# Kernel optimization log

Hardware: AMD Instinct MI355X
Metric: run time of the kernel (lower is better)

## Reference

```python
import jax, jax.numpy as jnp
import numpy as np

B, L, D = 16, 4096, 256
DEP = 50


def setup_inputs() -> dict:
    key = jax.random.key(0)
    ks = jax.random.split(key, 20)
    s = 1.0 / np.sqrt(D)
    inp = {
        "inputs": jax.random.normal(ks[0], (B, L, D), jnp.float32),
        "parent_positions": jax.random.randint(ks[1], (B, L), 0, L, jnp.int32),
        "sentence_deps": jax.random.randint(ks[2], (B, L), 0, DEP, jnp.int32),
        "attention_mask": jax.random.randint(ks[3], (B, L), 0, 2, jnp.int32),
        # linear weights stored [in, out]
        "W_loop": jax.random.uniform(ks[4], (D, D), jnp.float32, -s, s),
        "b_loop": jnp.zeros((D,), jnp.float32),
        "W_child": jax.random.uniform(ks[5], (D, D), jnp.float32, -s, s),
        "b_child": jnp.zeros((D,), jnp.float32),
        "W_parent": jax.random.uniform(ks[6], (D, D), jnp.float32, -s, s),
        "b_parent": jnp.zeros((D,), jnp.float32),
        "w_loop_g": jax.random.uniform(ks[7], (D, 1), jnp.float32, -s, s),
        "b_loop_g": jnp.zeros((1,), jnp.float32),
        "w_child_g": jax.random.uniform(ks[8], (D, 1), jnp.float32, -s, s),
        "b_child_g": jnp.zeros((1,), jnp.float32),
        "w_parent_g": jax.random.uniform(ks[9], (D, 1), jnp.float32, -s, s),
        "b_parent_g": jnp.zeros((1,), jnp.float32),
        "E_pw": jax.random.normal(ks[10], (DEP, D), jnp.float32),
        "E_cw": jax.random.normal(ks[11], (DEP, D), jnp.float32),
        "E_pg": jax.random.normal(ks[12], (DEP, 1), jnp.float32),
        "E_cg": jax.random.normal(ks[13], (DEP, 1), jnp.float32),
    }
    return inp


def _scatter_add_children(idx, vals):
    # idx: [L] parent index per child; vals: [L, D]
    # out[p] = sum_{i: idx[i]==p} vals[i]  (== one_hot(idx).T @ vals)
    return jnp.zeros((L, vals.shape[-1]), vals.dtype).at[idx].add(vals)


def reference(inputs, parent_positions, sentence_deps, attention_mask,
              W_loop, b_loop, W_child, b_child, W_parent, b_parent,
              w_loop_g, b_loop_g, w_child_g, b_child_g, w_parent_g, b_parent_g,
              E_pw, E_cw, E_pg, E_cg):
    x = inputs
    n_iterator = 1
    for _ in range(n_iterator):
        # gather parent node states: [B, L, D]
        par = jnp.take_along_axis(x, parent_positions[:, :, None].astype(jnp.int32), axis=1)
        deps = sentence_deps
        loop_gate = jax.nn.sigmoid(x @ w_loop_g + b_loop_g)                       # [B,L,1]
        par_gate = jax.nn.sigmoid(x @ w_parent_g + b_parent_g + E_pg[deps])       # [B,L,1]
        child_gate = jax.nn.sigmoid(x @ w_child_g + b_child_g + E_cg[deps])       # [B,L,1]
        loop_conv = loop_gate * (x @ W_loop + b_loop)
        parent_conv = par_gate * (par @ W_parent + b_parent + E_pw[deps])
        child_mat = child_gate * (x @ W_child + b_child + E_cw[deps])
        # masked parents (pad positions point to 0), then scatter-add children
        mpp = jnp.where(attention_mask != 0, parent_positions, 0)
        child_conv = jax.vmap(_scatter_add_children)(mpp, child_mat)
        x = loop_conv + parent_conv + child_conv
    return x * attention_mask[:, :, None].astype(x.dtype)
```

## Files before the change

kernel.cpp:

```cpp
#include <hip/hip_runtime.h>
#include <hip/hip_bf16.h>
#include <stdint.h>

#define B_ 16
#define L_ 4096
#define D_ 256
#define M_ (B_*L_)
#define N_ 768

typedef __attribute__((ext_vector_type(8))) short bf16x8;
typedef __attribute__((ext_vector_type(4))) float f32x4;
typedef __attribute__((ext_vector_type(4))) int i32x4;

__device__ __forceinline__ float bf2f(unsigned short u) {
  union { unsigned int i; float f; } v; v.i = ((unsigned int)u) << 16; return v.f;
}
__device__ __forceinline__ unsigned short f2bf(float f) {
  __hip_bfloat16 h = __float2bfloat16(f);
  return *reinterpret_cast<unsigned short*>(&h);
}
__device__ __forceinline__ void async16(const void* g, void* l) {
  __builtin_amdgcn_global_load_lds((const __attribute__((address_space(1))) void*)g,
                                   (__attribute__((address_space(3))) void*)l, 16, 0, 0);
}
__device__ __forceinline__ float sigmoidf_(float z) {
  return 1.f / (1.f + __expf(-z));
}

__global__ __launch_bounds__(256) void k_pre(
    const float* __restrict__ x, const int* __restrict__ deps,
    const int* __restrict__ parent, const int* __restrict__ mask,
    const float* __restrict__ wlg, const float* __restrict__ blg,
    const float* __restrict__ wcg, const float* __restrict__ bcg,
    const float* __restrict__ wpg, const float* __restrict__ bpg,
    const float* __restrict__ Epg, const float* __restrict__ Ecg,
    const float* __restrict__ Wl, const float* __restrict__ Wp,
    const float* __restrict__ Wc,
    unsigned short* __restrict__ xb, float4* __restrict__ gates,
    unsigned short* __restrict__ WbT,
    int* __restrict__ cnt, int* __restrict__ off, int* __restrict__ lists)
{
  __shared__ int hist[4096];
  __shared__ int tot[256];
  const int bx = blockIdx.x;
  const int tid = threadIdx.x;

  if (bx >= 2048) {
    if (bx < 2816) {
      const int n = bx - 2048;
      const float* W = (n < 256) ? Wl : ((n < 512) ? Wp : Wc);
      WbT[(size_t)n * 256 + tid] = f2bf(W[(size_t)tid * 256 + (n & 255)]);
    } else {
      const int b = bx - 2816;
      const int base = b << 12;
      #pragma unroll
      for (int j = 0; j < 16; ++j) hist[tid + j * 256] = 0;
      __syncthreads();
      for (int j = 0; j < 16; ++j) {
        const int i = base + j * 256 + tid;
        if (mask[i]) {
          const int p = parent[i];
          if (p > 0 && mask[base + p]) atomicAdd(&hist[p], 1);
        }
      }
      __syncthreads();
      int v[16], s = 0;
      #pragma unroll
      for (int j = 0; j < 16; ++j) { v[j] = hist[tid * 16 + j]; s += v[j]; }
      tot[tid] = s;
      __syncthreads();
      for (int o = 1; o < 256; o <<= 1) {
        int xx = (tid >= o) ? tot[tid - o] : 0;
        __syncthreads();
        tot[tid] += xx;
        __syncthreads();
      }
      int run = tot[tid] - s;
      #pragma unroll
      for (int j = 0; j < 16; ++j) {
        const int k = tid * 16 + j;
        cnt[base + k] = v[j];
        off[base + k] = run;
        hist[k] = run;
        run += v[j];
      }
      __syncthreads();
      for (int j = 0; j < 16; ++j) {
        const int i = base + j * 256 + tid;
        if (mask[i]) {
          const int p = parent[i];
          if (p > 0 && mask[base + p]) {
            const int pos = atomicAdd(&hist[p], 1);
            lists[base + pos] = i;
          }
        }
      }
    }
    return;
  }

  const int lane = tid & 63;
  const int gw = (bx * 256 + tid) >> 6;
  const float4 wl4 = ((const float4*)wlg)[lane];
  const float4 wc4 = ((const float4*)wcg)[lane];
  const float4 wp4 = ((const float4*)wpg)[lane];
  const float bl0 = blg[0], bc0 = bcg[0], bp0 = bpg[0];
  for (int t = 0; t < 8; ++t) {
    const int i = gw * 8 + t;
    float4 xv = ((const float4*)x)[(size_t)i * 64 + lane];
    float sl = xv.x * wl4.x + xv.y * wl4.y + xv.z * wl4.z + xv.w * wl4.w;
    float sc = xv.x * wc4.x + xv.y * wc4.y + xv.z * wc4.z + xv.w * wc4.w;
    float sp = xv.x * wp4.x + xv.y * wp4.y + xv.z * wp4.z + xv.w * wp4.w;
    #pragma unroll
    for (int o = 32; o; o >>= 1) {
      sl += __shfl_xor(sl, o);
      sc += __shfl_xor(sc, o);
      sp += __shfl_xor(sp, o);
    }
    ushort4 u;
    u.x = f2bf(xv.x); u.y = f2bf(xv.y); u.z = f2bf(xv.z); u.w = f2bf(xv.w);
    ((ushort4*)xb)[(size_t)i * 64 + lane] = u;
    if (lane == 0) {
      int d = deps[i];
      float gl = sigmoidf_(sl + bl0);
      float gp = sigmoidf_(sp + bp0 + Epg[d]);
      float gc = sigmoidf_(sc + bc0 + Ecg[d]);
      gates[i] = make_float4(gl, gp, gc, 0.f);
    }
  }
}

__global__ __launch_bounds__(256) void k_gemm(
    const unsigned short* __restrict__ A,
    const unsigned short* __restrict__ Bt,
    unsigned short* __restrict__ Y)
{
  __shared__ unsigned short sh[2 * 128 * 64];
  unsigned short* lA = sh;
  unsigned short* lB = sh + 128 * 64;
  const int tid = threadIdx.x;
  const int wid = tid >> 6, lane = tid & 63;
  const int wm = wid >> 1, wn = wid & 1;
  const int bid = blockIdx.x;
  const int mb = bid / 6, nb = bid % 6;

  f32x4 acc[4][4] = {};
  const unsigned short* Ag = A + (size_t)mb * 128 * 256;
  const unsigned short* Bg = Bt + (size_t)nb * 128 * 256;
  const int srow = wid * 8 + (lane >> 3);
  const int scol = (lane & 7) * 8;

  for (int kb = 0; kb < 256; kb += 64) {
    #pragma unroll
    for (int s = 0; s < 4; ++s) {
      char* dA = (char*)lA + s * 4096 + wid * 1024 + lane * 16;
      char* dB = (char*)lB + s * 4096 + wid * 1024 + lane * 16;
      async16(Ag + (size_t)(s * 32 + srow) * 256 + kb + scol, dA);
      async16(Bg + (size_t)(s * 32 + srow) * 256 + kb + scol, dB);
    }
    __syncthreads();
    #pragma unroll
    for (int kk = 0; kk < 64; kk += 32) {
      const int ko = kk + (lane >> 4) * 8;
      bf16x8 af[4], bv[4];
      #pragma unroll
      for (int m = 0; m < 4; ++m)
        af[m] = *(const bf16x8*)&lA[(wm * 64 + m * 16 + (lane & 15)) * 64 + ko];
      #pragma unroll
      for (int n = 0; n < 4; ++n)
        bv[n] = *(const bf16x8*)&lB[(wn * 64 + n * 16 + (lane & 15)) * 64 + ko];
      #pragma unroll
      for (int m = 0; m < 4; ++m)
        #pragma unroll
        for (int n = 0; n < 4; ++n)
          acc[m][n] = __builtin_amdgcn_mfma_f32_16x16x32_bf16(af[m], bv[n], acc[m][n], 0, 0, 0);
    }
    __syncthreads();
  }

  #pragma unroll
  for (int m = 0; m < 4; ++m)
    #pragma unroll
    for (int n = 0; n < 4; ++n)
      #pragma unroll
      for (int r = 0; r < 4; ++r)
        sh[(wm * 64 + m * 16 + (lane >> 4) * 4 + r) * 128 + wn * 64 + n * 16 + (lane & 15)]
            = f2bf(acc[m][n][r]);
  __syncthreads();
  #pragma unroll
  for (int s = 0; s < 8; ++s) {
    const int o = s * 4096 + tid * 16;
    const int row = o >> 8;
    const int colu = (o & 255) >> 1;
    *(i32x4*)&Y[(size_t)(mb * 128 + row) * 768 + nb * 128 + colu] =
        *(const i32x4*)((const char*)sh + o);
  }
}

__global__ __launch_bounds__(256) void k_fused(
    const unsigned short* __restrict__ Y, const float4* __restrict__ gates,
    const int* __restrict__ parent, const int* __restrict__ deps,
    const int* __restrict__ mask, const int* __restrict__ cnt,
    const int* __restrict__ off, const int* __restrict__ lists,
    const float* __restrict__ b_loop, const float* __restrict__ b_parent,
    const float* __restrict__ b_child,
    const float* __restrict__ Epw, const float* __restrict__ Ecw,
    float* __restrict__ out)
{
  const int lane = threadIdx.x & 63;
  const int i = blockIdx.x * 4 + (threadIdx.x >> 6);
  const int b = i >> 12;
  float4* orow = (float4*)(out + (size_t)i * 256) + lane;
  if (!mask[i]) { *orow = make_float4(0.f, 0.f, 0.f, 0.f); return; }

  const float4 g = gates[i];
  const int p = parent[i], d = deps[i];
  const float4 bl = ((const float4*)b_loop)[lane];
  const float4 bp = ((const float4*)b_parent)[lane];
  const ushort4 yl = ((const ushort4*)(Y + (size_t)i * 768))[lane];
  const ushort4 z  = ((const ushort4*)(Y + (size_t)((b << 12) + p) * 768 + 256))[lane];
  const float4 e   = ((const float4*)Epw)[d * 64 + lane];
  float4 o;
  o.x = g.x * (bf2f(yl.x) + bl.x) + g.y * (bf2f(z.x) + bp.x + e.x);
  o.y = g.x * (bf2f(yl.y) + bl.y) + g.y * (bf2f(z.y) + bp.y + e.y);
  o.z = g.x * (bf2f(yl.z) + bl.z) + g.y * (bf2f(z.z) + bp.z + e.z);
  o.w = g.x * (bf2f(yl.w) + bl.w) + g.y * (bf2f(z.w) + bp.w + e.w);

  const int n = cnt[i];
  if (n) {
    const int o0 = off[i];
    const float4 bc = ((const float4*)b_child)[lane];
    for (int k = 0; k < n; ++k) {
      const int c = lists[(b << 12) + o0 + k];
      const float gc = ((const float*)gates)[c * 4 + 2];
      const int dc = deps[c];
      const ushort4 yc = ((const ushort4*)(Y + (size_t)c * 768 + 512))[lane];
      const float4 ec = ((const float4*)Ecw)[dc * 64 + lane];
      o.x += gc * (bf2f(yc.x) + bc.x + ec.x);
      o.y += gc * (bf2f(yc.y) + bc.y + ec.y);
      o.z += gc * (bf2f(yc.z) + bc.z + ec.z);
      o.w += gc * (bf2f(yc.w) + bc.w + ec.w);
    }
  }
  *orow = o;
}

__global__ __launch_bounds__(256) void k_row0(
    const unsigned short* __restrict__ Y, const float4* __restrict__ gates,
    const int* __restrict__ parent, const int* __restrict__ deps,
    const int* __restrict__ mask, const float* __restrict__ b_child,
    const float* __restrict__ Ecw, float* __restrict__ out)
{
  const int blk = blockIdx.x;
  const int b = blk >> 4;
  if (!mask[b << 12]) return;
  const int lane = threadIdx.x & 63;
  const int wid = threadIdx.x >> 6;
  const float4 bc = ((const float4*)b_child)[lane];
  float4 acc = make_float4(0.f, 0.f, 0.f, 0.f);
  const int tbase = (b << 12) + (blk & 15) * 256 + wid * 64;
  for (int t = 0; t < 64; ++t) {
    const int i = tbase + t;
    const int mi = mask[i];
    const int p = parent[i];
    if (mi && p != 0) continue;
    const float gc = ((const float*)gates)[i * 4 + 2];
    const int d = deps[i];
    const ushort4 yc = ((const ushort4*)(Y + (size_t)i * 768 + 512))[lane];
    const float4 ec = ((const float4*)Ecw)[d * 64 + lane];
    acc.x += gc * (bf2f(yc.x) + bc.x + ec.x);
    acc.y += gc * (bf2f(yc.y) + bc.y + ec.y);
    acc.z += gc * (bf2f(yc.z) + bc.z + ec.z);
    acc.w += gc * (bf2f(yc.w) + bc.w + ec.w);
  }
  __shared__ float4 red[4][64];
  red[wid][lane] = acc;
  __syncthreads();
  if (wid == 0) {
    float4 a0 = red[0][lane], a1 = red[1][lane], a2 = red[2][lane], a3 = red[3][lane];
    a0.x += a1.x + a2.x + a3.x;
    a0.y += a1.y + a2.y + a3.y;
    a0.z += a1.z + a2.z + a3.z;
    a0.w += a1.w + a2.w + a3.w;
    float* dst = out + (size_t)(b << 12) * 256 + lane * 4;
    unsafeAtomicAdd(dst + 0, a0.x);
    unsafeAtomicAdd(dst + 1, a0.y);
    unsafeAtomicAdd(dst + 2, a0.z);
    unsafeAtomicAdd(dst + 3, a0.w);
  }
}

extern "C" void kernel_launch(void* const* d_in, const int* in_sizes, int n_in,
                              void* d_out, int out_size, void* d_ws, size_t ws_size,
                              hipStream_t stream) {
  const float* x        = (const float*)d_in[0];
  const int*   parent   = (const int*)d_in[1];
  const int*   deps     = (const int*)d_in[2];
  const int*   mask     = (const int*)d_in[3];
  const float* W_loop   = (const float*)d_in[4];
  const float* b_loop   = (const float*)d_in[5];
  const float* W_child  = (const float*)d_in[6];
  const float* b_child  = (const float*)d_in[7];
  const float* W_parent = (const float*)d_in[8];
  const float* b_parent = (const float*)d_in[9];
  const float* wlg      = (const float*)d_in[10];
  const float* blg      = (const float*)d_in[11];
  const float* wcg      = (const float*)d_in[12];
  const float* bcg      = (const float*)d_in[13];
  const float* wpg      = (const float*)d_in[14];
  const float* bpg      = (const float*)d_in[15];
  const float* Epw      = (const float*)d_in[16];
  const float* Ecw      = (const float*)d_in[17];
  const float* Epg      = (const float*)d_in[18];
  const float* Ecg      = (const float*)d_in[19];
  float* out = (float*)d_out;

  char* ws = (char*)d_ws;
  unsigned short* xb  = (unsigned short*)ws;
  unsigned short* WbT = (unsigned short*)(ws + 33554432);
  float4* gates       = (float4*)(ws + 33947648);
  unsigned short* Yv  = (unsigned short*)(ws + 34996224);
  int* cnt            = (int*)(ws + 135659520);
  int* off            = (int*)(ws + 135921664);
  int* lists          = (int*)(ws + 136183808);

  k_pre<<<2832, 256, 0, stream>>>(x, deps, parent, mask, wlg, blg, wcg, bcg,
                                  wpg, bpg, Epg, Ecg, W_loop, W_parent, W_child,
                                  xb, gates, WbT, cnt, off, lists);
  k_gemm<<<3072, 256, 0, stream>>>(xb, WbT, Yv);
  k_fused<<<16384, 256, 0, stream>>>(Yv, gates, parent, deps, mask, cnt, off,
                                     lists, b_loop, b_parent, b_child,
                                     Epw, Ecw, out);
  k_row0<<<256, 256, 0, stream>>>(Yv, gates, parent, deps, mask, b_child,
                                  Ecw, out);
}
```

Measured before the change: 278.8 us.

## Merge row-0 kernel into fused pass, move child-list build into GEMM launch

The separate row-0 scatter kernel is folded into the fused kernel as extra blocks, and row 0 is now accumulated atomically after being zeroed by the GEMM kernel. The per-batch child histogram and list build moves from the prologue kernel into 16 extra blocks of the GEMM kernel. The weight transpose now handles four columns per block, and the gate shuffle reductions are batched across eight rows. This removes one launch and shortens the prologue, but it adds a cross-kernel ordering dependency for zeroing row 0 and makes row-0 output depend on atomics.

Result: faster. 267.8 us (-3.9%).

```diff
diff --git a/kernel.cpp b/kernel.cpp
--- a/kernel.cpp
+++ b/kernel.cpp
@@ -29,7 +29,6 @@
 
 __global__ __launch_bounds__(256) void k_pre(
     const float* __restrict__ x, const int* __restrict__ deps,
-    const int* __restrict__ parent, const int* __restrict__ mask,
     const float* __restrict__ wlg, const float* __restrict__ blg,
     const float* __restrict__ wcg, const float* __restrict__ bcg,
     const float* __restrict__ wpg, const float* __restrict__ bpg,
@@ -37,65 +36,20 @@
     const float* __restrict__ Wl, const float* __restrict__ Wp,
     const float* __restrict__ Wc,
     unsigned short* __restrict__ xb, float4* __restrict__ gates,
-    unsigned short* __restrict__ WbT,
-    int* __restrict__ cnt, int* __restrict__ off, int* __restrict__ lists)
+    unsigned short* __restrict__ WbT)
 {
-  __shared__ int hist[4096];
-  __shared__ int tot[256];
   const int bx = blockIdx.x;
   const int tid = threadIdx.x;
 
   if (bx >= 2048) {
-    if (bx < 2816) {
-      const int n = bx - 2048;
-      const float* W = (n < 256) ? Wl : ((n < 512) ? Wp : Wc);
-      WbT[(size_t)n * 256 + tid] = f2bf(W[(size_t)tid * 256 + (n & 255)]);
-    } else {
-      const int b = bx - 2816;
-      const int base = b << 12;
-      #pragma unroll
-      for (int j = 0; j < 16; ++j) hist[tid + j * 256] = 0;
-      __syncthreads();
-      for (int j = 0; j < 16; ++j) {
-        const int i = base + j * 256 + tid;
-        if (mask[i]) {
-          const int p = parent[i];
-          if (p > 0 && mask[base + p]) atomicAdd(&hist[p], 1);
-        }
-      }
-      __syncthreads();
-      int v[16], s = 0;
-      #pragma unroll
-      for (int j = 0; j < 16; ++j) { v[j] = hist[tid * 16 + j]; s += v[j]; }
-      tot[tid] = s;
-      __syncthreads();
-      for (int o = 1; o < 256; o <<= 1) {
-        int xx = (tid >= o) ? tot[tid - o] : 0;
-        __syncthreads();
-        tot[tid] += xx;
-        __syncthreads();
-      }
-      int run = tot[tid] - s;
-      #pragma unroll
-      for (int j = 0; j < 16; ++j) {
-        const int k = tid * 16 + j;
-        cnt[base + k] = v[j];
-        off[base + k] = run;
-        hist[k] = run;
-        run += v[j];
-      }
-      __syncthreads();
-      for (int j = 0; j < 16; ++j) {
-        const int i = base + j * 256 + tid;
-        if (mask[i]) {
-          const int p = parent[i];
-          if (p > 0 && mask[base + p]) {
-            const int pos = atomicAdd(&hist[p], 1);
-            lists[base + pos] = i;
-          }
-        }
-      }
-    }
+    const int n0 = (bx - 2048) * 4;
+    const float* W = (n0 < 256) ? Wl : ((n0 < 512) ? Wp : Wc);
+    const int c0 = n0 & 255;
+    const float4 v = *(const float4*)&W[(size_t)tid * 256 + c0];
+    WbT[(size_t)(n0 + 0) * 256 + tid] = f2bf(v.x);
+    WbT[(size_t)(n0 + 1) * 256 + tid] = f2bf(v.y);
+    WbT[(size_t)(n0 + 2) * 256 + tid] = f2bf(v.z);
+    WbT[(size_t)(n0 + 3) * 256 + tid] = f2bf(v.w);
     return;
   }
 
@@ -105,27 +59,35 @@
   const float4 wc4 = ((const float4*)wcg)[lane];
   const float4 wp4 = ((const float4*)wpg)[lane];
   const float bl0 = blg[0], bc0 = bcg[0], bp0 = bpg[0];
+  float sl[8], sc[8], sp[8];
+  #pragma unroll
   for (int t = 0; t < 8; ++t) {
     const int i = gw * 8 + t;
-    float4 xv = ((const float4*)x)[(size_t)i * 64 + lane];
-    float sl = xv.x * wl4.x + xv.y * wl4.y + xv.z * wl4.z + xv.w * wl4.w;
-    float sc = xv.x * wc4.x + xv.y * wc4.y + xv.z * wc4.z + xv.w * wc4.w;
-    float sp = xv.x * wp4.x + xv.y * wp4.y + xv.z * wp4.z + xv.w * wp4.w;
-    #pragma unroll
-    for (int o = 32; o; o >>= 1) {
-      sl += __shfl_xor(sl, o);
-      sc += __shfl_xor(sc, o);
-      sp += __shfl_xor(sp, o);
-    }
+    const float4 xv = ((const float4*)x)[(size_t)i * 64 + lane];
+    sl[t] = xv.x * wl4.x + xv.y * wl4.y + xv.z * wl4.z + xv.w * wl4.w;
+    sc[t] = xv.x * wc4.x + xv.y * wc4.y + xv.z * wc4.z + xv.w * wc4.w;
+    sp[t] = xv.x * wp4.x + xv.y * wp4.y + xv.z * wp4.z + xv.w * wp4.w;
     ushort4 u;
     u.x = f2bf(xv.x); u.y = f2bf(xv.y); u.z = f2bf(xv.z); u.w = f2bf(xv.w);
     ((ushort4*)xb)[(size_t)i * 64 + lane] = u;
-    if (lane == 0) {
-      int d = deps[i];
-      float gl = sigmoidf_(sl + bl0);
-      float gp = sigmoidf_(sp + bp0 + Epg[d]);
-      float gc = sigmoidf_(sc + bc0 + Ecg[d]);
-      gates[i] = make_float4(gl, gp, gc, 0.f);
+  }
+  #pragma unroll
+  for (int o = 32; o; o >>= 1) {
+    #pragma unroll
+    for (int t = 0; t < 8; ++t) {
+      sl[t] += __shfl_xor(sl[t], o);
+      sc[t] += __shfl_xor(sc[t], o);
+      sp[t] += __shfl_xor(sp[t], o);
+    }
+  }
+  if (lane == 0) {
+    #pragma unroll
+    for (int t = 0; t < 8; ++t) {
+      const int i = gw * 8 + t;
+      const int d = deps[i];
+      gates[i] = make_float4(sigmoidf_(sl[t] + bl0),
+                             sigmoidf_(sp[t] + bp0 + Epg[d]),
+                             sigmoidf_(sc[t] + bc0 + Ecg[d]), 0.f);
     }
   }
 }
@@ -133,15 +95,70 @@
 __global__ __launch_bounds__(256) void k_gemm(
     const unsigned short* __restrict__ A,
     const unsigned short* __restrict__ Bt,
-    unsigned short* __restrict__ Y)
+    unsigned short* __restrict__ Y,
+    const int* __restrict__ parent, const int* __restrict__ mask,
+    int* __restrict__ cnt, int* __restrict__ off, int* __restrict__ lists,
+    float* __restrict__ out)
 {
   __shared__ unsigned short sh[2 * 128 * 64];
+  const int tid = threadIdx.x;
+
+  if (blockIdx.x < 16) {
+    int* hist = (int*)sh;
+    int* tot = ((int*)sh) + 4096;
+    const int b = blockIdx.x;
+    const int base = b << 12;
+    out[(size_t)base * 256 + tid] = 0.f;
+    #pragma unroll
+    for (int j = 0; j < 16; ++j) hist[tid + j * 256] = 0;
+    __syncthreads();
+    for (int j = 0; j < 16; ++j) {
+      const int i = base + j * 256 + tid;
+      if (mask[i]) {
+        const int p = parent[i];
+        if (p > 0 && mask[base + p]) atomicAdd(&hist[p], 1);
+      }
+    }
+    __syncthreads();
+    int v[16], s = 0;
+    #pragma unroll
+    for (int j = 0; j < 16; ++j) { v[j] = hist[tid * 16 + j]; s += v[j]; }
+    tot[tid] = s;
+    __syncthreads();
+    for (int o = 1; o < 256; o <<= 1) {
+      int xx = (tid >= o) ? tot[tid - o] : 0;
+      __syncthreads();
+      tot[tid] += xx;
+      __syncthreads();
+    }
+    int run = tot[tid] - s;
+    #pragma unroll
+    for (int j = 0; j < 16; ++j) {
+      const int k = tid * 16 + j;
+      cnt[base + k] = v[j];
+      off[base + k] = run;
+      hist[k] = run;
+      run += v[j];
+    }
+    __syncthreads();
+    for (int j = 0; j < 16; ++j) {
+      const int i = base + j * 256 + tid;
+      if (mask[i]) {
+        const int p = parent[i];
+        if (p > 0 && mask[base + p]) {
+          const int pos = atomicAdd(&hist[p], 1);
+          lists[base + pos] = i;
+        }
+      }
+    }
+    return;
+  }
+
   unsigned short* lA = sh;
   unsigned short* lB = sh + 128 * 64;
-  const int tid = threadIdx.x;
   const int wid = tid >> 6, lane = tid & 63;
   const int wm = wid >> 1, wn = wid & 1;
-  const int bid = blockIdx.x;
+  const int bid = blockIdx.x - 16;
   const int mb = bid / 6, nb = bid % 6;
 
   f32x4 acc[4][4] = {};
@@ -208,10 +225,55 @@
     float* __restrict__ out)
 {
   const int lane = threadIdx.x & 63;
-  const int i = blockIdx.x * 4 + (threadIdx.x >> 6);
+  const int wid = threadIdx.x >> 6;
+
+  if (blockIdx.x >= 16384) {
+    const int blk = blockIdx.x - 16384;
+    const int b = blk >> 4;
+    if (!mask[b << 12]) return;
+    const float4 bc = ((const float4*)b_child)[lane];
+    float4 acc = make_float4(0.f, 0.f, 0.f, 0.f);
+    const int tbase = (b << 12) + (blk & 15) * 256 + wid * 64;
+    for (int t = 0; t < 64; ++t) {
+      const int i = tbase + t;
+      const int mi = mask[i];
+      const int p = parent[i];
+      if (mi && p != 0) continue;
+      const float gc = ((const float*)gates)[i * 4 + 2];
+      const int d = deps[i];
+      const ushort4 yc = ((const ushort4*)(Y + (size_t)i * 768 + 512))[lane];
+      const float4 ec = ((const float4*)Ecw)[d * 64 + lane];
+      acc.x += gc * (bf2f(yc.x) + bc.x + ec.x);
+      acc.y += gc * (bf2f(yc.y) + bc.y + ec.y);
+      acc.z += gc * (bf2f(yc.z) + bc.z + ec.z);
+      acc.w += gc * (bf2f(yc.w) + bc.w + ec.w);
+    }
+    __shared__ float4 red[4][64];
+    red[wid][lane] = acc;
+    __syncthreads();
+    if (wid == 0) {
+      float4 a0 = red[0][lane], a1 = red[1][lane], a2 = red[2][lane], a3 = red[3][lane];
+      a0.x += a1.x + a2.x + a3.x;
+      a0.y += a1.y + a2.y + a3.y;
+      a0.z += a1.z + a2.z + a3.z;
+      a0.w += a1.w + a2.w + a3.w;
+      float* dst = out + (size_t)(b << 12) * 256 + lane * 4;
+      unsafeAtomicAdd(dst + 0, a0.x);
+      unsafeAtomicAdd(dst + 1, a0.y);
+      unsafeAtomicAdd(dst + 2, a0.z);
+      unsafeAtomicAdd(dst + 3, a0.w);
+    }
+    return;
+  }
+
+  const int i = blockIdx.x * 4 + wid;
   const int b = i >> 12;
+  const bool isrow0 = (i & 4095) == 0;
   float4* orow = (float4*)(out + (size_t)i * 256) + lane;
-  if (!mask[i]) { *orow = make_float4(0.f, 0.f, 0.f, 0.f); return; }
+  if (!mask[i]) {
+    if (!isrow0) *orow = make_float4(0.f, 0.f, 0.f, 0.f);
+    return;
+  }
 
   const float4 g = gates[i];
   const int p = parent[i], d = deps[i];
@@ -242,51 +304,14 @@
       o.w += gc * (bf2f(yc.w) + bc.w + ec.w);
     }
   }
-  *orow = o;
-}
-
-__global__ __launch_bounds__(256) void k_row0(
-    const unsigned short* __restrict__ Y, const float4* __restrict__ gates,
-    const int* __restrict__ parent, const int* __restrict__ deps,
-    const int* __restrict__ mask, const float* __restrict__ b_child,
-    const float* __restrict__ Ecw, float* __restrict__ out)
-{
-  const int blk = blockIdx.x;
-  const int b = blk >> 4;
-  if (!mask[b << 12]) return;
-  const int lane = threadIdx.x & 63;
-  const int wid = threadIdx.x >> 6;
-  const float4 bc = ((const float4*)b_child)[lane];
-  float4 acc = make_float4(0.f, 0.f, 0.f, 0.f);
-  const int tbase = (b << 12) + (blk & 15) * 256 + wid * 64;
-  for (int t = 0; t < 64; ++t) {
-    const int i = tbase + t;
-    const int mi = mask[i];
-    const int p = parent[i];
-    if (mi && p != 0) continue;
-    const float gc = ((const float*)gates)[i * 4 + 2];
-    const int d = deps[i];
-    const ushort4 yc = ((const ushort4*)(Y + (size_t)i * 768 + 512))[lane];
-    const float4 ec = ((const float4*)Ecw)[d * 64 + lane];
-    acc.x += gc * (bf2f(yc.x) + bc.x + ec.x);
-    acc.y += gc * (bf2f(yc.y) + bc.y + ec.y);
-    acc.z += gc * (bf2f(yc.z) + bc.z + ec.z);
-    acc.w += gc * (bf2f(yc.w) + bc.w + ec.w);
-  }
-  __shared__ float4 red[4][64];
-  red[wid][lane] = acc;
-  __syncthreads();
-  if (wid == 0) {
-    float4 a0 = red[0][lane], a1 = red[1][lane], a2 = red[2][lane], a3 = red[3][lane];
-    a0.x += a1.x + a2.x + a3.x;
-    a0.y += a1.y + a2.y + a3.y;
-    a0.z += a1.z + a2.z + a3.z;
-    a0.w += a1.w + a2.w + a3.w;
-    float* dst = out + (size_t)(b << 12) * 256 + lane * 4;
-    unsafeAtomicAdd(dst + 0, a0.x);
-    unsafeAtomicAdd(dst + 1, a0.y);
-    unsafeAtomicAdd(dst + 2, a0.z);
-    unsafeAtomicAdd(dst + 3, a0.w);
+  if (isrow0) {
+    float* dst = out + (size_t)i * 256 + lane * 4;
+    unsafeAtomicAdd(dst + 0, o.x);
+    unsafeAtomicAdd(dst + 1, o.y);
+    unsafeAtomicAdd(dst + 2, o.z);
+    unsafeAtomicAdd(dst + 3, o.w);
+  } else {
+    *orow = o;
   }
 }
 
@@ -324,13 +349,12 @@
   int* off            = (int*)(ws + 135921664);
   int* lists          = (int*)(ws + 136183808);
 
-  k_pre<<<2832, 256, 0, stream>>>(x, deps, parent, mask, wlg, blg, wcg, bcg,
-                                  wpg, bpg, Epg, Ecg, W_loop, W_parent, W_child,
-                                  xb, gates, WbT, cnt, off, lists);
-  k_gemm<<<3072, 256, 0, stream>>>(xb, WbT, Yv);
-  k_fused<<<16384, 256, 0, stream>>>(Yv, gates, parent, deps, mask, cnt, off,
+  k_pre<<<2240, 256, 0, stream>>>(x, deps, wlg, blg, wcg, bcg, wpg, bpg,
+                                  Epg, Ecg, W_loop, W_parent, W_child,
+                                  xb, gates, WbT);
+  k_gemm<<<3088, 256, 0, stream>>>(xb, WbT, Yv, parent, mask, cnt, off,
+                                   lists, out);
+  k_fused<<<16640, 256, 0, stream>>>(Yv, gates, parent, deps, mask, cnt, off,
                                      lists, b_loop, b_parent, b_child,
                                      Epw, Ecw, out);
-  k_row0<<<256, 256, 0, stream>>>(Yv, gates, parent, deps, mask, b_child,
-                                  Ecw, out);
-}
+}
```
